# Kernel optimization log

Measured on AMD Instinct MI355X. Metric: run time of the kernel, lower is better.

The kernel has to match this reference:

```python
import jax, jax.numpy as jnp
import numpy as np

B, T, C, H = 2, 2048, 1024, 16
HD = C // H  # head_dim = 64

def _rope(x, cos, sin):
    # x: [B,H,T,HD]; cos/sin: [T,HD//2]
    x2 = x.reshape(*x.shape[:-1], HD // 2, 2)
    x0, x1 = x2[..., 0], x2[..., 1]
    # complex multiply (x0 + i x1) * (cos + i sin)
    o0 = x0 * cos - x1 * sin
    o1 = x0 * sin + x1 * cos
    return jnp.stack([o0, o1], axis=-1).reshape(x.shape)

def setup_inputs() -> dict:
    key = jax.random.key(0)
    k1, k2, k3 = jax.random.split(key, 3)
    x = jax.random.normal(k1, (B, T, C), dtype=jnp.float32)
    w_qkv = jax.random.normal(k2, (C, 3 * C), dtype=jnp.float32) * (1.0 / np.sqrt(C))
    w_proj = jax.random.normal(k3, (C, C), dtype=jnp.float32) * (1.0 / np.sqrt(C))
    # standard RoPE frequencies: theta_j = 10000^(-2j/HD), angles t*theta_j
    inv_freq = 1.0 / (10000.0 ** (np.arange(0, HD, 2, dtype=np.float32) / HD))  # [HD//2]
    ang = np.arange(T, dtype=np.float32)[:, None] * inv_freq[None, :]           # [T,HD//2]
    return {"x": x, "w_qkv": w_qkv, "w_proj": w_proj,
            "freqs_cos": jnp.asarray(np.cos(ang)), "freqs_sin": jnp.asarray(np.sin(ang))}

def reference(x, w_qkv, w_proj, freqs_cos, freqs_sin):
    qkv = x @ w_qkv                                   # [B,T,3C]
    q, k, v = jnp.split(qkv, 3, axis=-1)
    def heads(t):
        return t.reshape(B, T, H, HD).transpose(0, 2, 1, 3)  # [B,H,T,HD]
    q, k, v = heads(q), heads(k), heads(v)
    q = _rope(q, freqs_cos, freqs_sin)
    k = _rope(k, freqs_cos, freqs_sin)
    scores = jnp.einsum('bhqd,bhkd->bhqk', q, k) * (1.0 / np.sqrt(HD))
    causal = jnp.tril(jnp.ones((T, T), dtype=bool))
    scores = jnp.where(causal, scores, jnp.finfo(scores.dtype).min)
    attn = jax.nn.softmax(scores, axis=-1)
    y = jnp.einsum('bhqk,bhkd->bhqd', attn, v)        # [B,H,T,HD]
    y = y.transpose(0, 2, 1, 3).reshape(B, T, C)
    return y @ w_proj
```

## Files before the change

### kernel.cpp

```cpp
#include <hip/hip_runtime.h>

typedef float  floatx4 __attribute__((ext_vector_type(4)));
typedef _Float16 half8 __attribute__((ext_vector_type(8)));
typedef _Float16 half4v __attribute__((ext_vector_type(4)));
typedef _Float16 half2v __attribute__((ext_vector_type(2)));

__device__ __forceinline__ void gld16(const void* g, void* l) {
    __builtin_amdgcn_global_load_lds(
        (const __attribute__((address_space(1))) void*)g,
        (__attribute__((address_space(3))) void*)l, 16, 0, 0);
}

__global__ __launch_bounds__(256) void conv_x_kernel(const float* __restrict__ x,
                                                     _Float16* __restrict__ xh) {
    int i = blockIdx.x * 256 + threadIdx.x;
    float4 v = ((const float4*)x)[i];
    half4v o = { (_Float16)v.x, (_Float16)v.y, (_Float16)v.z, (_Float16)v.w };
    ((half4v*)xh)[i] = o;
}

__global__ __launch_bounds__(256) void transpose_f32f16(const float* __restrict__ W,
                                                        _Float16* __restrict__ WT,
                                                        int K, int N) {
    __shared__ _Float16 t[64][72];
    int n0 = blockIdx.x * 64, k0 = blockIdx.y * 64;
    int c = threadIdx.x & 63, r4 = threadIdx.x >> 6;
    for (int rr = 0; rr < 64; rr += 4) {
        int k = k0 + rr + r4;
        t[rr + r4][c] = (_Float16)W[(size_t)k * N + n0 + c];
    }
    __syncthreads();
    for (int rr = 0; rr < 64; rr += 4) {
        int n = n0 + rr + r4;
        WT[(size_t)n * K + k0 + c] = t[c][rr + r4];
    }
}

__global__ __launch_bounds__(256) void gemm_tn(const _Float16* __restrict__ A,
                                               const _Float16* __restrict__ BT,
                                               _Float16* __restrict__ Cf16,
                                               float* __restrict__ Cf32,
                                               int M, int N, int K) {
    __shared__ __align__(16) _Float16 sAB[2 * 128 * 32];
    _Float16* sA = sAB;
    _Float16* sB = sAB + 128 * 32;

    const int tid  = threadIdx.x;
    const int wave = tid >> 6, lane = tid & 63;
    const int lrow = lane & 15, quad = lane >> 4;
    const int bm = blockIdx.x * 128, bn = blockIdx.y * 128;
    const int waveM = (wave >> 1) * 64, waveN = (wave & 1) * 64;

    floatx4 acc[4][4] = {};

    const int r0 = tid >> 2,          k80 = (tid & 3) * 8;
    const int r1 = (tid + 256) >> 2,  k81 = ((tid + 256) & 3) * 8;
    _Float16* lA0 = sA + (wave * 64) * 8;
    _Float16* lA1 = sA + (wave * 64 + 256) * 8;
    _Float16* lB0 = sB + (wave * 64) * 8;
    _Float16* lB1 = sB + (wave * 64 + 256) * 8;
    const _Float16* A0 = A + (size_t)(bm + r0) * K + k80;
    const _Float16* A1 = A + (size_t)(bm + r1) * K + k81;
    const _Float16* B0 = BT + (size_t)(bn + r0) * K + k80;
    const _Float16* B1 = BT + (size_t)(bn + r1) * K + k81;

    for (int k0 = 0; k0 < K; k0 += 32) {
        gld16(A0 + k0, lA0);
        gld16(A1 + k0, lA1);
        gld16(B0 + k0, lB0);
        gld16(B1 + k0, lB1);
        __syncthreads();

        half8 aF[4], bF[4];
#pragma unroll
        for (int mt = 0; mt < 4; ++mt)
            aF[mt] = *(const half8*)&sA[(waveM + mt * 16 + lrow) * 32 + quad * 8];
#pragma unroll
        for (int nt = 0; nt < 4; ++nt)
            bF[nt] = *(const half8*)&sB[(waveN + nt * 16 + lrow) * 32 + quad * 8];
#pragma unroll
        for (int mt = 0; mt < 4; ++mt)
#pragma unroll
            for (int nt = 0; nt < 4; ++nt)
                acc[mt][nt] = __builtin_amdgcn_mfma_f32_16x16x32_f16(
                    aF[mt], bF[nt], acc[mt][nt], 0, 0, 0);
        __syncthreads();
    }

    if (Cf16) {
        const int PS = 132;
#pragma unroll
        for (int pass = 0; pass < 4; ++pass) {
            if ((wave >> 1) == (pass >> 1)) {
#pragma unroll
                for (int mt2 = 0; mt2 < 2; ++mt2) {
                    int mt = (pass & 1) * 2 + mt2;
#pragma unroll
                    for (int nt = 0; nt < 4; ++nt)
#pragma unroll
                        for (int r = 0; r < 4; ++r)
                            sAB[(mt2 * 16 + quad * 4 + r) * PS + waveN + nt * 16 + lrow] =
                                (_Float16)acc[mt][nt][r];
                }
            }
            __syncthreads();
            {
                int row = tid >> 3, c0 = (tid & 7) * 16;
                const uint4* src = (const uint4*)&sAB[row * PS + c0];
                uint4 d0 = src[0], d1 = src[1];
                uint4* dst = (uint4*)&Cf16[(size_t)(bm + pass * 32 + row) * N + bn + c0];
                dst[0] = d0; dst[1] = d1;
            }
            __syncthreads();
        }
    } else {
#pragma unroll
        for (int mt = 0; mt < 4; ++mt)
#pragma unroll
            for (int nt = 0; nt < 4; ++nt)
#pragma unroll
                for (int r = 0; r < 4; ++r) {
                    int row = bm + waveM + mt * 16 + quad * 4 + r;
                    int col = bn + waveN + nt * 16 + lrow;
                    Cf32[(size_t)row * N + col] = acc[mt][nt][r];
                }
    }
}

__global__ __launch_bounds__(256) void rope_split(const _Float16* __restrict__ qkv,
                                                  const float* __restrict__ fc,
                                                  const float* __restrict__ fs,
                                                  _Float16* __restrict__ qh,
                                                  _Float16* __restrict__ kh) {
    int row = blockIdx.x;
    int b = row >> 11, t = row & 2047;
    const _Float16* src = qkv + (size_t)row * 3072;
    for (int p = threadIdx.x; p < 512; p += 256) {
        int h = p >> 5, j = p & 31;
        float c = fc[t * 32 + j], s = fs[t * 32 + j];
        size_t o = ((size_t)(b * 16 + h) * 2048 + t) * 64 + 2 * j;
        {
            half2v xin = *(const half2v*)&src[h * 64 + 2 * j];
            float x0 = (float)xin[0], x1 = (float)xin[1];
            half2v out = { (_Float16)(x0 * c - x1 * s), (_Float16)(x0 * s + x1 * c) };
            *(half2v*)&qh[o] = out;
        }
        {
            half2v xin = *(const half2v*)&src[1024 + h * 64 + 2 * j];
            float x0 = (float)xin[0], x1 = (float)xin[1];
            half2v out = { (_Float16)(x0 * c - x1 * s), (_Float16)(x0 * s + x1 * c) };
            *(half2v*)&kh[o] = out;
        }
    }
}

__global__ __launch_bounds__(256) void vtrans(const _Float16* __restrict__ qkv,
                                              _Float16* __restrict__ vt) {
    __shared__ _Float16 s[64][72];
    int bh = blockIdx.y, t0 = blockIdx.x * 64;
    int b = bh >> 4, h = bh & 15;
    int c = threadIdx.x & 63, r4 = threadIdx.x >> 6;
    const _Float16* src = qkv + 2048 + h * 64;
    for (int rr = 0; rr < 64; rr += 4) {
        int t = t0 + rr + r4;
        s[rr + r4][c] = src[(size_t)(b * 2048 + t) * 3072 + c];
    }
    __syncthreads();
    for (int rr = 0; rr < 64; rr += 4) {
        int hd = rr + r4;
        vt[((size_t)bh * 64 + hd) * 2048 + t0 + c] = s[c][hd];
    }
}

__global__ __launch_bounds__(256) void attn_lazy(const _Float16* __restrict__ Q,
                                                 const _Float16* __restrict__ Kk,
                                                 const _Float16* __restrict__ Vt,
                                                 _Float16* __restrict__ Y) {
    __shared__ __align__(16) _Float16 sK[2][64 * 64];
    __shared__ __align__(16) _Float16 sV[2][64 * 64];
    __shared__ __align__(16) _Float16 sP[64 * 72];

    const int bh = blockIdx.y, b = bh >> 4, h = bh & 15;
    const int qt = 31 - (int)blockIdx.x;
    const int q0 = qt * 64;
    const int tid = threadIdx.x;
    const int wave = tid >> 6, lane = tid & 63;
    const int lq = lane & 15, quad = lane >> 4;

    const _Float16* Kbase = Kk + (size_t)bh * 2048 * 64;
    const _Float16* Vbase = Vt + (size_t)bh * 64 * 2048;

    const _Float16 qscale = (_Float16)(0.125f * 1.44269504f);
    half8 qF[2];
    {
        const _Float16* Qp = Q + ((size_t)bh * 2048 + q0 + wave * 16 + lq) * 64;
#pragma unroll
        for (int ks = 0; ks < 2; ++ks)
            qF[ks] = (*(const half8*)(Qp + ks * 32 + quad * 8)) * qscale;
    }

    floatx4 O[4] = {};
    float lpart = 0.f;

    auto stage = [&](int bufi, int kt) {
        const _Float16* kb = Kbase + (size_t)kt * 64 * 64;
        const _Float16* vb = Vbase + kt * 64;
        _Float16* dK = sK[bufi];
        _Float16* dV = sV[bufi];
#pragma unroll
        for (int hlf = 0; hlf < 2; ++hlf) {
            int s = tid + hlf * 256;
            int row = s >> 3;
            int ccg = (s & 7) ^ (row & 7);
            gld16(kb + row * 64 + ccg * 8, dK + s * 8);
        }
#pragma unroll
        for (int hlf = 0; hlf < 2; ++hlf) {
            int s = tid + hlf * 256;
            int row = s >> 3;
            int ccg = (s & 7) ^ (row & 7);
            gld16(vb + (size_t)row * 2048 + ccg * 8, dV + s * 8);
        }
    };

    stage(0, 0);
    __syncthreads();

    for (int it = 0; it <= qt; ++it) {
        int cur = it & 1;
        if (it < qt) stage(cur ^ 1, it + 1);
        const _Float16* bK = sK[cur];
        const _Float16* bV = sV[cur];

        floatx4 St[4];
#pragma unroll
        for (int kt4 = 0; kt4 < 4; ++kt4) {
            floatx4 s = { -12.f, -12.f, -12.f, -12.f };
#pragma unroll
            for (int ks = 0; ks < 2; ++ks) {
                half8 kf = *(const half8*)&bK[(kt4 * 16 + lq) * 64 +
                                              (((ks * 4 + quad) ^ (lq & 7)) * 8)];
                s = __builtin_amdgcn_mfma_f32_16x16x32_f16(kf, qF[ks], s, 0, 0, 0);
            }
            St[kt4] = s;
        }
        if (it == qt) {
#pragma unroll
            for (int kt4 = 0; kt4 < 4; ++kt4)
#pragma unroll
                for (int r = 0; r < 4; ++r)
                    if (kt4 * 16 + quad * 4 + r > wave * 16 + lq) St[kt4][r] = -1e30f;
        }
#pragma unroll
        for (int kt4 = 0; kt4 < 4; ++kt4)
#pragma unroll
            for (int r = 0; r < 4; ++r)
                St[kt4][r] = __builtin_amdgcn_exp2f(St[kt4][r]);
        lpart += (St[0][0] + St[0][1] + St[0][2] + St[0][3])
               + (St[1][0] + St[1][1] + St[1][2] + St[1][3])
               + (St[2][0] + St[2][1] + St[2][2] + St[2][3])
               + (St[3][0] + St[3][1] + St[3][2] + St[3][3]);

        _Float16* pw = (_Float16*)&sP[(wave * 16 + lq) * 72];
#pragma unroll
        for (int kt4 = 0; kt4 < 4; ++kt4) {
            half4v pk = { (_Float16)St[kt4][0], (_Float16)St[kt4][1],
                          (_Float16)St[kt4][2], (_Float16)St[kt4][3] };
            *(half4v*)(pw + kt4 * 16 + quad * 4) = pk;
        }
        half8 aP[2];
#pragma unroll
        for (int ks = 0; ks < 2; ++ks)
            aP[ks] = *(const half8*)(pw + ks * 32 + quad * 8);
#pragma unroll
        for (int nt = 0; nt < 4; ++nt)
#pragma unroll
            for (int ks = 0; ks < 2; ++ks) {
                half8 vf = *(const half8*)&bV[(nt * 16 + lq) * 64 +
                                              (((ks * 4 + quad) ^ (lq & 7)) * 8)];
                O[nt] = __builtin_amdgcn_mfma_f32_16x16x32_f16(aP[ks], vf, O[nt], 0, 0, 0);
            }
        __syncthreads();
    }

    float l = lpart;
    l += __shfl_xor(l, 16);
    l += __shfl_xor(l, 32);
    float invl = 1.0f / l;
#pragma unroll
    for (int r = 0; r < 4; ++r) {
        float iv = __shfl(invl, (lane & 48) | (quad * 4 + r));
        int q = q0 + wave * 16 + quad * 4 + r;
        size_t rowoff = ((size_t)b * 2048 + q) * 1024 + h * 64;
#pragma unroll
        for (int nt = 0; nt < 4; ++nt)
            Y[rowoff + nt * 16 + lq] = (_Float16)(O[nt][r] * iv);
    }
}

extern "C" void kernel_launch(void* const* d_in, const int* in_sizes, int n_in,
                              void* d_out, int out_size, void* d_ws, size_t ws_size,
                              hipStream_t stream) {
    const float* x     = (const float*)d_in[0];
    const float* wqkv  = (const float*)d_in[1];
    const float* wproj = (const float*)d_in[2];
    const float* fc    = (const float*)d_in[3];
    const float* fs    = (const float*)d_in[4];
    float* out = (float*)d_out;

    char* ws = (char*)d_ws;
    _Float16* xh   = (_Float16*)(ws);
    _Float16* wqT  = (_Float16*)(ws + ((size_t)8  << 20));
    _Float16* wpT  = (_Float16*)(ws + ((size_t)14 << 20));
    _Float16* qkvh = (_Float16*)(ws + ((size_t)16 << 20));
    _Float16* qh   = (_Float16*)(ws + ((size_t)40 << 20));
    _Float16* kh   = (_Float16*)(ws + ((size_t)48 << 20));
    _Float16* vt   = (_Float16*)(ws + ((size_t)56 << 20));
    _Float16* yh   = xh;

    conv_x_kernel<<<4096, 256, 0, stream>>>(x, xh);
    transpose_f32f16<<<dim3(48, 16), 256, 0, stream>>>(wqkv, wqT, 1024, 3072);
    transpose_f32f16<<<dim3(16, 16), 256, 0, stream>>>(wproj, wpT, 1024, 1024);
    gemm_tn<<<dim3(32, 24), 256, 0, stream>>>(xh, wqT, qkvh, nullptr, 4096, 3072, 1024);
    rope_split<<<4096, 256, 0, stream>>>(qkvh, fc, fs, qh, kh);
    vtrans<<<dim3(32, 32), 256, 0, stream>>>(qkvh, vt);
    attn_lazy<<<dim3(32, 32), 256, 0, stream>>>(qh, kh, vt, yh);
    gemm_tn<<<dim3(32, 8), 256, 0, stream>>>(yh, wpT, nullptr, out, 4096, 1024, 1024);
}
```

Baseline: 232.7 us.

## Pair causal query tiles per block, fuse RoPE with V transpose

Each attention block now handles two query tiles (t and 31-t), which balances causal work across blocks and lets both tiles reuse each staged K/V tile. The P matrix now stays in registers and is fed to 16x16x16 MFMAs, so the LDS round trip for P is gone. RoPE and the V transpose are merged into one kernel, saving a launch and a pass over qkv. In exchange the grid is halved to 512 blocks, which may lower occupancy, and each thread holds more registers for the two sets of accumulators.

Result: faster. 216.4 us (-7.0%).

```diff
diff --git a/kernel.cpp b/kernel.cpp
--- a/kernel.cpp
+++ b/kernel.cpp
@@ -127,62 +127,67 @@
     }
 }
 
-__global__ __launch_bounds__(256) void rope_split(const _Float16* __restrict__ qkv,
-                                                  const float* __restrict__ fc,
-                                                  const float* __restrict__ fs,
-                                                  _Float16* __restrict__ qh,
-                                                  _Float16* __restrict__ kh) {
-    int row = blockIdx.x;
-    int b = row >> 11, t = row & 2047;
-    const _Float16* src = qkv + (size_t)row * 3072;
-    for (int p = threadIdx.x; p < 512; p += 256) {
-        int h = p >> 5, j = p & 31;
-        float c = fc[t * 32 + j], s = fs[t * 32 + j];
-        size_t o = ((size_t)(b * 16 + h) * 2048 + t) * 64 + 2 * j;
-        {
-            half2v xin = *(const half2v*)&src[h * 64 + 2 * j];
-            float x0 = (float)xin[0], x1 = (float)xin[1];
-            half2v out = { (_Float16)(x0 * c - x1 * s), (_Float16)(x0 * s + x1 * c) };
-            *(half2v*)&qh[o] = out;
-        }
-        {
-            half2v xin = *(const half2v*)&src[1024 + h * 64 + 2 * j];
-            float x0 = (float)xin[0], x1 = (float)xin[1];
-            half2v out = { (_Float16)(x0 * c - x1 * s), (_Float16)(x0 * s + x1 * c) };
-            *(half2v*)&kh[o] = out;
-        }
-    }
-}
-
-__global__ __launch_bounds__(256) void vtrans(const _Float16* __restrict__ qkv,
-                                              _Float16* __restrict__ vt) {
+__global__ __launch_bounds__(256) void rope_vt(const _Float16* __restrict__ qkv,
+                                               const float* __restrict__ fc,
+                                               const float* __restrict__ fs,
+                                               _Float16* __restrict__ qh,
+                                               _Float16* __restrict__ kh,
+                                               _Float16* __restrict__ vt) {
     __shared__ _Float16 s[64][72];
-    int bh = blockIdx.y, t0 = blockIdx.x * 64;
-    int b = bh >> 4, h = bh & 15;
-    int c = threadIdx.x & 63, r4 = threadIdx.x >> 6;
-    const _Float16* src = qkv + 2048 + h * 64;
-    for (int rr = 0; rr < 64; rr += 4) {
-        int t = t0 + rr + r4;
-        s[rr + r4][c] = src[(size_t)(b * 2048 + t) * 3072 + c];
-    }
-    __syncthreads();
-    for (int rr = 0; rr < 64; rr += 4) {
-        int hd = rr + r4;
-        vt[((size_t)bh * 64 + hd) * 2048 + t0 + c] = s[c][hd];
-    }
-}
-
-__global__ __launch_bounds__(256) void attn_lazy(const _Float16* __restrict__ Q,
-                                                 const _Float16* __restrict__ Kk,
-                                                 const _Float16* __restrict__ Vt,
-                                                 _Float16* __restrict__ Y) {
+    const int bh = blockIdx.y, b = bh >> 4, h = bh & 15;
+    const int t0 = blockIdx.x * 64;
+    const int tid = threadIdx.x;
+
+    {
+        int c4 = (tid & 15) * 4;
+        int j0 = c4 >> 1;
+        int rr = tid >> 4;
+#pragma unroll
+        for (int pass = 0; pass < 4; ++pass) {
+            int tt = t0 + pass * 16 + rr;
+            const _Float16* src = qkv + (size_t)(b * 2048 + tt) * 3072 + h * 64 + c4;
+            float c0 = fc[tt * 32 + j0],     s0 = fs[tt * 32 + j0];
+            float c1 = fc[tt * 32 + j0 + 1], s1 = fs[tt * 32 + j0 + 1];
+            half4v qv = *(const half4v*)(src);
+            half4v kv = *(const half4v*)(src + 1024);
+            half4v qo, ko;
+            {
+                float x0 = (float)qv[0], x1 = (float)qv[1];
+                qo[0] = (_Float16)(x0 * c0 - x1 * s0); qo[1] = (_Float16)(x0 * s0 + x1 * c0);
+                x0 = (float)qv[2]; x1 = (float)qv[3];
+                qo[2] = (_Float16)(x0 * c1 - x1 * s1); qo[3] = (_Float16)(x0 * s1 + x1 * c1);
+                x0 = (float)kv[0]; x1 = (float)kv[1];
+                ko[0] = (_Float16)(x0 * c0 - x1 * s0); ko[1] = (_Float16)(x0 * s0 + x1 * c0);
+                x0 = (float)kv[2]; x1 = (float)kv[3];
+                ko[2] = (_Float16)(x0 * c1 - x1 * s1); ko[3] = (_Float16)(x0 * s1 + x1 * c1);
+            }
+            size_t o = ((size_t)bh * 2048 + tt) * 64 + c4;
+            *(half4v*)&qh[o] = qo;
+            *(half4v*)&kh[o] = ko;
+        }
+    }
+    {
+        int c = tid & 63, r4 = tid >> 6;
+        const _Float16* srcv = qkv + 2048 + h * 64;
+        for (int rr = 0; rr < 64; rr += 4)
+            s[rr + r4][c] = srcv[(size_t)(b * 2048 + t0 + rr + r4) * 3072 + c];
+        __syncthreads();
+        for (int rr = 0; rr < 64; rr += 4)
+            vt[((size_t)bh * 64 + rr + r4) * 2048 + t0 + c] = s[c][rr + r4];
+    }
+}
+
+__global__ __launch_bounds__(256) void attn_fused(const _Float16* __restrict__ Q,
+                                                  const _Float16* __restrict__ Kk,
+                                                  const _Float16* __restrict__ Vt,
+                                                  _Float16* __restrict__ Y) {
     __shared__ __align__(16) _Float16 sK[2][64 * 64];
     __shared__ __align__(16) _Float16 sV[2][64 * 64];
-    __shared__ __align__(16) _Float16 sP[64 * 72];
 
     const int bh = blockIdx.y, b = bh >> 4, h = bh & 15;
-    const int qt = 31 - (int)blockIdx.x;
-    const int q0 = qt * 64;
+    const int t = blockIdx.x;
+    const int qt0 = t, qt1 = 31 - t;
+    const int nst = qt1 + 1;
     const int tid = threadIdx.x;
     const int wave = tid >> 6, lane = tid & 63;
     const int lq = lane & 15, quad = lane >> 4;
@@ -191,16 +196,19 @@
     const _Float16* Vbase = Vt + (size_t)bh * 64 * 2048;
 
     const _Float16 qscale = (_Float16)(0.125f * 1.44269504f);
-    half8 qF[2];
-    {
-        const _Float16* Qp = Q + ((size_t)bh * 2048 + q0 + wave * 16 + lq) * 64;
-#pragma unroll
-        for (int ks = 0; ks < 2; ++ks)
-            qF[ks] = (*(const half8*)(Qp + ks * 32 + quad * 8)) * qscale;
-    }
-
-    floatx4 O[4] = {};
-    float lpart = 0.f;
+    half8 qF[2][2];
+    {
+        const _Float16* Qp0 = Q + ((size_t)bh * 2048 + qt0 * 64 + wave * 16 + lq) * 64;
+        const _Float16* Qp1 = Q + ((size_t)bh * 2048 + qt1 * 64 + wave * 16 + lq) * 64;
+#pragma unroll
+        for (int ks = 0; ks < 2; ++ks) {
+            qF[0][ks] = (*(const half8*)(Qp0 + ks * 32 + quad * 8)) * qscale;
+            qF[1][ks] = (*(const half8*)(Qp1 + ks * 32 + quad * 8)) * qscale;
+        }
+    }
+
+    floatx4 O0[4] = {}, O1[4] = {};
+    float lp0 = 0.f, lp1 = 0.f;
 
     auto stage = [&](int bufi, int kt) {
         const _Float16* kb = Kbase + (size_t)kt * 64 * 64;
@@ -226,75 +234,108 @@
     stage(0, 0);
     __syncthreads();
 
-    for (int it = 0; it <= qt; ++it) {
+    for (int it = 0; it < nst; ++it) {
         int cur = it & 1;
-        if (it < qt) stage(cur ^ 1, it + 1);
+        if (it + 1 < nst) stage(cur ^ 1, it + 1);
         const _Float16* bK = sK[cur];
         const _Float16* bV = sV[cur];
-
-        floatx4 St[4];
+        const bool do0 = (it <= qt0);
+
+        floatx4 S0[4], S1[4];
 #pragma unroll
         for (int kt4 = 0; kt4 < 4; ++kt4) {
-            floatx4 s = { -12.f, -12.f, -12.f, -12.f };
-#pragma unroll
-            for (int ks = 0; ks < 2; ++ks) {
-                half8 kf = *(const half8*)&bK[(kt4 * 16 + lq) * 64 +
-                                              (((ks * 4 + quad) ^ (lq & 7)) * 8)];
-                s = __builtin_amdgcn_mfma_f32_16x16x32_f16(kf, qF[ks], s, 0, 0, 0);
-            }
-            St[kt4] = s;
-        }
-        if (it == qt) {
+            half8 kf0 = *(const half8*)&bK[(kt4 * 16 + lq) * 64 + ((quad ^ (lq & 7)) * 8)];
+            half8 kf1 = *(const half8*)&bK[(kt4 * 16 + lq) * 64 + (((4 + quad) ^ (lq & 7)) * 8)];
+            floatx4 a1 = { -12.f, -12.f, -12.f, -12.f };
+            a1 = __builtin_amdgcn_mfma_f32_16x16x32_f16(kf0, qF[1][0], a1, 0, 0, 0);
+            a1 = __builtin_amdgcn_mfma_f32_16x16x32_f16(kf1, qF[1][1], a1, 0, 0, 0);
+            S1[kt4] = a1;
+            if (do0) {
+                floatx4 a0 = { -12.f, -12.f, -12.f, -12.f };
+                a0 = __builtin_amdgcn_mfma_f32_16x16x32_f16(kf0, qF[0][0], a0, 0, 0, 0);
+                a0 = __builtin_amdgcn_mfma_f32_16x16x32_f16(kf1, qF[0][1], a0, 0, 0, 0);
+                S0[kt4] = a0;
+            }
+        }
+        if (it == qt1) {
 #pragma unroll
             for (int kt4 = 0; kt4 < 4; ++kt4)
 #pragma unroll
                 for (int r = 0; r < 4; ++r)
-                    if (kt4 * 16 + quad * 4 + r > wave * 16 + lq) St[kt4][r] = -1e30f;
-        }
-#pragma unroll
-        for (int kt4 = 0; kt4 < 4; ++kt4)
+                    if (kt4 * 16 + quad * 4 + r > wave * 16 + lq) S1[kt4][r] = -1e30f;
+        }
+        if (do0 && it == qt0) {
+#pragma unroll
+            for (int kt4 = 0; kt4 < 4; ++kt4)
+#pragma unroll
+                for (int r = 0; r < 4; ++r)
+                    if (kt4 * 16 + quad * 4 + r > wave * 16 + lq) S0[kt4][r] = -1e30f;
+        }
+        half4v P0[4], P1[4];
+#pragma unroll
+        for (int kt4 = 0; kt4 < 4; ++kt4) {
 #pragma unroll
             for (int r = 0; r < 4; ++r)
-                St[kt4][r] = __builtin_amdgcn_exp2f(St[kt4][r]);
-        lpart += (St[0][0] + St[0][1] + St[0][2] + St[0][3])
-               + (St[1][0] + St[1][1] + St[1][2] + St[1][3])
-               + (St[2][0] + St[2][1] + St[2][2] + St[2][3])
-               + (St[3][0] + St[3][1] + St[3][2] + St[3][3]);
-
-        _Float16* pw = (_Float16*)&sP[(wave * 16 + lq) * 72];
-#pragma unroll
-        for (int kt4 = 0; kt4 < 4; ++kt4) {
-            half4v pk = { (_Float16)St[kt4][0], (_Float16)St[kt4][1],
-                          (_Float16)St[kt4][2], (_Float16)St[kt4][3] };
-            *(half4v*)(pw + kt4 * 16 + quad * 4) = pk;
-        }
-        half8 aP[2];
-#pragma unroll
-        for (int ks = 0; ks < 2; ++ks)
-            aP[ks] = *(const half8*)(pw + ks * 32 + quad * 8);
-#pragma unroll
-        for (int nt = 0; nt < 4; ++nt)
-#pragma unroll
-            for (int ks = 0; ks < 2; ++ks) {
-                half8 vf = *(const half8*)&bV[(nt * 16 + lq) * 64 +
-                                              (((ks * 4 + quad) ^ (lq & 7)) * 8)];
-                O[nt] = __builtin_amdgcn_mfma_f32_16x16x32_f16(aP[ks], vf, O[nt], 0, 0, 0);
-            }
+                S1[kt4][r] = __builtin_amdgcn_exp2f(S1[kt4][r]);
+            lp1 += S1[kt4][0] + S1[kt4][1] + S1[kt4][2] + S1[kt4][3];
+            P1[kt4] = half4v{ (_Float16)S1[kt4][0], (_Float16)S1[kt4][1],
+                              (_Float16)S1[kt4][2], (_Float16)S1[kt4][3] };
+        }
+        if (do0) {
+#pragma unroll
+            for (int kt4 = 0; kt4 < 4; ++kt4) {
+#pragma unroll
+                for (int r = 0; r < 4; ++r)
+                    S0[kt4][r] = __builtin_amdgcn_exp2f(S0[kt4][r]);
+                lp0 += S0[kt4][0] + S0[kt4][1] + S0[kt4][2] + S0[kt4][3];
+                P0[kt4] = half4v{ (_Float16)S0[kt4][0], (_Float16)S0[kt4][1],
+                                  (_Float16)S0[kt4][2], (_Float16)S0[kt4][3] };
+            }
+        }
+#pragma unroll
+        for (int nt = 0; nt < 4; ++nt) {
+#pragma unroll
+            for (int kt4 = 0; kt4 < 4; ++kt4) {
+                half4v vf = *(const half4v*)&bV[(nt * 16 + lq) * 64 +
+                                                (((kt4 * 2 + (quad >> 1)) ^ (lq & 7)) * 8) +
+                                                (quad & 1) * 4];
+                O1[nt] = __builtin_amdgcn_mfma_f32_16x16x16f16(P1[kt4], vf, O1[nt], 0, 0, 0);
+                if (do0)
+                    O0[nt] = __builtin_amdgcn_mfma_f32_16x16x16f16(P0[kt4], vf, O0[nt], 0, 0, 0);
+            }
+        }
         __syncthreads();
     }
 
-    float l = lpart;
-    l += __shfl_xor(l, 16);
-    l += __shfl_xor(l, 32);
-    float invl = 1.0f / l;
-#pragma unroll
-    for (int r = 0; r < 4; ++r) {
-        float iv = __shfl(invl, (lane & 48) | (quad * 4 + r));
-        int q = q0 + wave * 16 + quad * 4 + r;
-        size_t rowoff = ((size_t)b * 2048 + q) * 1024 + h * 64;
-#pragma unroll
-        for (int nt = 0; nt < 4; ++nt)
-            Y[rowoff + nt * 16 + lq] = (_Float16)(O[nt][r] * iv);
+    {
+        float l = lp0;
+        l += __shfl_xor(l, 16);
+        l += __shfl_xor(l, 32);
+        float invl = 1.0f / l;
+#pragma unroll
+        for (int r = 0; r < 4; ++r) {
+            float iv = __shfl(invl, (lane & 48) | (quad * 4 + r));
+            int q = qt0 * 64 + wave * 16 + quad * 4 + r;
+            size_t rowoff = ((size_t)b * 2048 + q) * 1024 + h * 64;
+#pragma unroll
+            for (int nt = 0; nt < 4; ++nt)
+                Y[rowoff + nt * 16 + lq] = (_Float16)(O0[nt][r] * iv);
+        }
+    }
+    {
+        float l = lp1;
+        l += __shfl_xor(l, 16);
+        l += __shfl_xor(l, 32);
+        float invl = 1.0f / l;
+#pragma unroll
+        for (int r = 0; r < 4; ++r) {
+            float iv = __shfl(invl, (lane & 48) | (quad * 4 + r));
+            int q = qt1 * 64 + wave * 16 + quad * 4 + r;
+            size_t rowoff = ((size_t)b * 2048 + q) * 1024 + h * 64;
+#pragma unroll
+            for (int nt = 0; nt < 4; ++nt)
+                Y[rowoff + nt * 16 + lq] = (_Float16)(O1[nt][r] * iv);
+        }
     }
 }
 
@@ -322,8 +363,7 @@
     transpose_f32f16<<<dim3(48, 16), 256, 0, stream>>>(wqkv, wqT, 1024, 3072);
     transpose_f32f16<<<dim3(16, 16), 256, 0, stream>>>(wproj, wpT, 1024, 1024);
     gemm_tn<<<dim3(32, 24), 256, 0, stream>>>(xh, wqT, qkvh, nullptr, 4096, 3072, 1024);
-    rope_split<<<4096, 256, 0, stream>>>(qkvh, fc, fs, qh, kh);
-    vtrans<<<dim3(32, 32), 256, 0, stream>>>(qkvh, vt);
-    attn_lazy<<<dim3(32, 32), 256, 0, stream>>>(qh, kh, vt, yh);
+    rope_vt<<<dim3(32, 32), 256, 0, stream>>>(qkvh, fc, fs, qh, kh, vt);
+    attn_fused<<<dim3(16, 32), 256, 0, stream>>>(qh, kh, vt, yh);
     gemm_tn<<<dim3(32, 8), 256, 0, stream>>>(yh, wpT, nullptr, out, 4096, 1024, 1024);
 }
```

## Pair causal query tiles per block for load balance and fuse RoPE with V transpose

Applied to the files above, without the earlier changes.

The attention kernel now assigns each 512-thread block two query tiles, p and 31-p, which share every K/V stage load. Each wave's 16 MFMA rows mix 8 rows from each tile, so per-block work is balanced across the causal triangle and staged K/V are reused by twice as many queries. RoPE and the V transpose are merged into one kernel with vectorized half4 accesses, saving a launch. The cost is extra masking on every iteration from qt0 onward, where keys past the short tile's queries are computed and then discarded.

After: 215.9 us. 7.2% less time.

```diff
diff --git a/kernel.cpp b/kernel.cpp
--- a/kernel.cpp
+++ b/kernel.cpp
@@ -127,73 +127,81 @@
     }
 }
 
-__global__ __launch_bounds__(256) void rope_split(const _Float16* __restrict__ qkv,
-                                                  const float* __restrict__ fc,
-                                                  const float* __restrict__ fs,
-                                                  _Float16* __restrict__ qh,
-                                                  _Float16* __restrict__ kh) {
-    int row = blockIdx.x;
-    int b = row >> 11, t = row & 2047;
-    const _Float16* src = qkv + (size_t)row * 3072;
-    for (int p = threadIdx.x; p < 512; p += 256) {
-        int h = p >> 5, j = p & 31;
-        float c = fc[t * 32 + j], s = fs[t * 32 + j];
-        size_t o = ((size_t)(b * 16 + h) * 2048 + t) * 64 + 2 * j;
-        {
-            half2v xin = *(const half2v*)&src[h * 64 + 2 * j];
-            float x0 = (float)xin[0], x1 = (float)xin[1];
-            half2v out = { (_Float16)(x0 * c - x1 * s), (_Float16)(x0 * s + x1 * c) };
-            *(half2v*)&qh[o] = out;
-        }
-        {
-            half2v xin = *(const half2v*)&src[1024 + h * 64 + 2 * j];
-            float x0 = (float)xin[0], x1 = (float)xin[1];
-            half2v out = { (_Float16)(x0 * c - x1 * s), (_Float16)(x0 * s + x1 * c) };
-            *(half2v*)&kh[o] = out;
-        }
-    }
-}
-
-__global__ __launch_bounds__(256) void vtrans(const _Float16* __restrict__ qkv,
-                                              _Float16* __restrict__ vt) {
+__global__ __launch_bounds__(256) void rope_vt(const _Float16* __restrict__ qkv,
+                                               const float* __restrict__ fc,
+                                               const float* __restrict__ fs,
+                                               _Float16* __restrict__ qh,
+                                               _Float16* __restrict__ kh,
+                                               _Float16* __restrict__ vt) {
     __shared__ _Float16 s[64][72];
-    int bh = blockIdx.y, t0 = blockIdx.x * 64;
-    int b = bh >> 4, h = bh & 15;
-    int c = threadIdx.x & 63, r4 = threadIdx.x >> 6;
-    const _Float16* src = qkv + 2048 + h * 64;
-    for (int rr = 0; rr < 64; rr += 4) {
-        int t = t0 + rr + r4;
-        s[rr + r4][c] = src[(size_t)(b * 2048 + t) * 3072 + c];
-    }
-    __syncthreads();
-    for (int rr = 0; rr < 64; rr += 4) {
-        int hd = rr + r4;
-        vt[((size_t)bh * 64 + hd) * 2048 + t0 + c] = s[c][hd];
-    }
-}
-
-__global__ __launch_bounds__(256) void attn_lazy(const _Float16* __restrict__ Q,
-                                                 const _Float16* __restrict__ Kk,
-                                                 const _Float16* __restrict__ Vt,
-                                                 _Float16* __restrict__ Y) {
+    const int bh = blockIdx.y, b = bh >> 4, h = bh & 15;
+    const int t0 = blockIdx.x * 64;
+    const int tid = threadIdx.x;
+
+    {
+        int c4 = (tid & 15) * 4;
+        int j0 = c4 >> 1;
+        int rr = tid >> 4;
+#pragma unroll
+        for (int pass = 0; pass < 4; ++pass) {
+            int tt = t0 + pass * 16 + rr;
+            const _Float16* src = qkv + (size_t)(b * 2048 + tt) * 3072 + h * 64 + c4;
+            float c0 = fc[tt * 32 + j0],     s0 = fs[tt * 32 + j0];
+            float c1 = fc[tt * 32 + j0 + 1], s1 = fs[tt * 32 + j0 + 1];
+            half4v qv = *(const half4v*)(src);
+            half4v kv = *(const half4v*)(src + 1024);
+            half4v qo, ko;
+            {
+                float x0 = (float)qv[0], x1 = (float)qv[1];
+                qo[0] = (_Float16)(x0 * c0 - x1 * s0); qo[1] = (_Float16)(x0 * s0 + x1 * c0);
+                x0 = (float)qv[2]; x1 = (float)qv[3];
+                qo[2] = (_Float16)(x0 * c1 - x1 * s1); qo[3] = (_Float16)(x0 * s1 + x1 * c1);
+                x0 = (float)kv[0]; x1 = (float)kv[1];
+                ko[0] = (_Float16)(x0 * c0 - x1 * s0); ko[1] = (_Float16)(x0 * s0 + x1 * c0);
+                x0 = (float)kv[2]; x1 = (float)kv[3];
+                ko[2] = (_Float16)(x0 * c1 - x1 * s1); ko[3] = (_Float16)(x0 * s1 + x1 * c1);
+            }
+            size_t o = ((size_t)bh * 2048 + tt) * 64 + c4;
+            *(half4v*)&qh[o] = qo;
+            *(half4v*)&kh[o] = ko;
+        }
+    }
+    {
+        int c = tid & 63, r4 = tid >> 6;
+        const _Float16* srcv = qkv + 2048 + h * 64;
+        for (int rr = 0; rr < 64; rr += 4)
+            s[rr + r4][c] = srcv[(size_t)(b * 2048 + t0 + rr + r4) * 3072 + c];
+        __syncthreads();
+        for (int rr = 0; rr < 64; rr += 4)
+            vt[((size_t)bh * 64 + rr + r4) * 2048 + t0 + c] = s[c][rr + r4];
+    }
+}
+
+__global__ __launch_bounds__(512, 4) void attn_mix(const _Float16* __restrict__ Q,
+                                                   const _Float16* __restrict__ Kk,
+                                                   const _Float16* __restrict__ Vt,
+                                                   _Float16* __restrict__ Y) {
     __shared__ __align__(16) _Float16 sK[2][64 * 64];
     __shared__ __align__(16) _Float16 sV[2][64 * 64];
-    __shared__ __align__(16) _Float16 sP[64 * 72];
+    __shared__ __align__(16) _Float16 sP[128 * 72];
 
     const int bh = blockIdx.y, b = bh >> 4, h = bh & 15;
-    const int qt = 31 - (int)blockIdx.x;
-    const int q0 = qt * 64;
+    const int p = blockIdx.x;
+    const int qt0 = p, qt1 = 31 - p;
+    const int nst = qt1 + 1;
     const int tid = threadIdx.x;
     const int wave = tid >> 6, lane = tid & 63;
     const int lq = lane & 15, quad = lane >> 4;
 
+    const int qglob = (lq < 8 ? qt0 * 64 : qt1 * 64) + wave * 8 + (lq & 7);
+
     const _Float16* Kbase = Kk + (size_t)bh * 2048 * 64;
     const _Float16* Vbase = Vt + (size_t)bh * 64 * 2048;
 
     const _Float16 qscale = (_Float16)(0.125f * 1.44269504f);
     half8 qF[2];
     {
-        const _Float16* Qp = Q + ((size_t)bh * 2048 + q0 + wave * 16 + lq) * 64;
+        const _Float16* Qp = Q + ((size_t)bh * 2048 + qglob) * 64;
 #pragma unroll
         for (int ks = 0; ks < 2; ++ks)
             qF[ks] = (*(const half8*)(Qp + ks * 32 + quad * 8)) * qscale;
@@ -205,30 +213,19 @@
     auto stage = [&](int bufi, int kt) {
         const _Float16* kb = Kbase + (size_t)kt * 64 * 64;
         const _Float16* vb = Vbase + kt * 64;
-        _Float16* dK = sK[bufi];
-        _Float16* dV = sV[bufi];
-#pragma unroll
-        for (int hlf = 0; hlf < 2; ++hlf) {
-            int s = tid + hlf * 256;
-            int row = s >> 3;
-            int ccg = (s & 7) ^ (row & 7);
-            gld16(kb + row * 64 + ccg * 8, dK + s * 8);
-        }
-#pragma unroll
-        for (int hlf = 0; hlf < 2; ++hlf) {
-            int s = tid + hlf * 256;
-            int row = s >> 3;
-            int ccg = (s & 7) ^ (row & 7);
-            gld16(vb + (size_t)row * 2048 + ccg * 8, dV + s * 8);
-        }
+        int s = tid;
+        int row = s >> 3;
+        int ccg = (s & 7) ^ (row & 7);
+        gld16(kb + row * 64 + ccg * 8, sK[bufi] + s * 8);
+        gld16(vb + (size_t)row * 2048 + ccg * 8, sV[bufi] + s * 8);
     };
 
     stage(0, 0);
     __syncthreads();
 
-    for (int it = 0; it <= qt; ++it) {
+    for (int it = 0; it < nst; ++it) {
         int cur = it & 1;
-        if (it < qt) stage(cur ^ 1, it + 1);
+        if (it + 1 < nst) stage(cur ^ 1, it + 1);
         const _Float16* bK = sK[cur];
         const _Float16* bV = sV[cur];
 
@@ -244,12 +241,13 @@
             }
             St[kt4] = s;
         }
-        if (it == qt) {
+        if (it >= qt0) {
+            int keybase = it * 64;
 #pragma unroll
             for (int kt4 = 0; kt4 < 4; ++kt4)
 #pragma unroll
                 for (int r = 0; r < 4; ++r)
-                    if (kt4 * 16 + quad * 4 + r > wave * 16 + lq) St[kt4][r] = -1e30f;
+                    if (keybase + kt4 * 16 + quad * 4 + r > qglob) St[kt4][r] = -1e30f;
         }
 #pragma unroll
         for (int kt4 = 0; kt4 < 4; ++kt4)
@@ -289,9 +287,10 @@
     float invl = 1.0f / l;
 #pragma unroll
     for (int r = 0; r < 4; ++r) {
-        float iv = __shfl(invl, (lane & 48) | (quad * 4 + r));
-        int q = q0 + wave * 16 + quad * 4 + r;
-        size_t rowoff = ((size_t)b * 2048 + q) * 1024 + h * 64;
+        int m = quad * 4 + r;
+        float iv = __shfl(invl, (lane & 48) | m);
+        int qrow = (m < 8 ? qt0 * 64 : qt1 * 64) + wave * 8 + (m & 7);
+        size_t rowoff = ((size_t)b * 2048 + qrow) * 1024 + h * 64;
 #pragma unroll
         for (int nt = 0; nt < 4; ++nt)
             Y[rowoff + nt * 16 + lq] = (_Float16)(O[nt][r] * iv);
@@ -322,8 +321,7 @@
     transpose_f32f16<<<dim3(48, 16), 256, 0, stream>>>(wqkv, wqT, 1024, 3072);
     transpose_f32f16<<<dim3(16, 16), 256, 0, stream>>>(wproj, wpT, 1024, 1024);
     gemm_tn<<<dim3(32, 24), 256, 0, stream>>>(xh, wqT, qkvh, nullptr, 4096, 3072, 1024);
-    rope_split<<<4096, 256, 0, stream>>>(qkvh, fc, fs, qh, kh);
-    vtrans<<<dim3(32, 32), 256, 0, stream>>>(qkvh, vt);
-    attn_lazy<<<dim3(32, 32), 256, 0, stream>>>(qh, kh, vt, yh);
+    rope_vt<<<dim3(32, 32), 256, 0, stream>>>(qkvh, fc, fs, qh, kh, vt);
+    attn_mix<<<dim3(16, 32), 512, 0, stream>>>(qh, kh, vt, yh);
     gemm_tn<<<dim3(32, 8), 256, 0, stream>>>(yh, wpT, nullptr, out, 4096, 1024, 1024);
 }
```
